# Kernel tuning notes

Measured on AMD Instinct MI355X. Metric: run time of the kernel, lower is better.

The kernel has to match this reference:

```python
import jax, jax.numpy as jnp
import numpy as np

B, N = 64, 4096          # trees per batch, leaves per complete binary tree
V, S = 21, 50            # amino-acid vocab, grammar-symbol vocab
E, H = 64, 128           # embed_dim, hidden_dim


def setup_inputs() -> dict:
    key = jax.random.key(0)
    ks = jax.random.split(key, 16)

    def lin_w(k, din, dout):
        return (jax.random.normal(k, (dout, din), jnp.float32) / np.sqrt(din)).astype(jnp.float32)

    tokens = jax.random.randint(ks[0], (B, N), 0, V, dtype=jnp.int32)
    symbols = jax.random.randint(ks[1], (B, N - 1), 0, S, dtype=jnp.int32)

    emb = jax.random.normal(ks[2], (V, E), jnp.float32) * 0.02
    emb = emb.at[0].set(0.0)  # padding_idx=0
    sym_emb = jax.random.normal(ks[3], (S, E), jnp.float32) * 0.02

    return {
        "tokens": tokens, "symbols": symbols,
        "emb": emb, "sym_emb": sym_emb,
        "Wp": lin_w(ks[4], E, H), "bp": jnp.zeros((H,), jnp.float32),
        "Wi": lin_w(ks[5], H, H), "bi": jnp.zeros((H,), jnp.float32),
        "Ui": lin_w(ks[6], H, H),
        "Wf": lin_w(ks[7], H, H), "bf": jnp.zeros((H,), jnp.float32),
        "Uf": lin_w(ks[8], H, H),
        "Wo": lin_w(ks[9], H, H), "bo": jnp.zeros((H,), jnp.float32),
        "Uo": lin_w(ks[10], H, H),
        "Wu": lin_w(ks[11], H, H), "bu": jnp.zeros((H,), jnp.float32),
        "Uu": lin_w(ks[12], H, H),
        "Wout": lin_w(ks[13], H, H), "bout": jnp.zeros((H,), jnp.float32),
    }


def _encode(tokens, symbols, emb, sym_emb, Wp, bp, Wi, bi, Ui, Wf, bf, Uf,
            Wo, bo, Uo, Wu, bu, Uu, Wout, bout):
    emb = emb.at[0].set(0.0)  # padding row contributes nothing (and gets no grad)

    # Leaf nodes: amino-acid embedding -> input_proj, no children.
    x = emb[tokens] @ Wp.T + bp                      # [B, N, H]
    i = jax.nn.sigmoid(x @ Wi.T + bi)
    o = jax.nn.sigmoid(x @ Wo.T + bo)
    u = jnp.tanh(x @ Wu.T + bu)
    c = i * u                                        # [B, N, H]
    h = o * jnp.tanh(c)

    # Bottom-up over levels of the complete binary tree (Child-Sum Tree-LSTM).
    off, n = 0, N
    while n > 1:
        m = n // 2
        xs = sym_emb[symbols[:, off:off + m]] @ Wp.T + bp   # [B, m, H]
        hl, hr = h[:, 0::2], h[:, 1::2]
        cl, cr = c[:, 0::2], c[:, 1::2]
        ht = hl + hr                                         # h_tilde = sum_j h_j
        gi = jax.nn.sigmoid(xs @ Wi.T + bi + ht @ Ui.T)
        go = jax.nn.sigmoid(xs @ Wo.T + bo + ht @ Uo.T)
        gu = jnp.tanh(xs @ Wu.T + bu + ht @ Uu.T)
        fx = xs @ Wf.T + bf
        fl = jax.nn.sigmoid(fx + hl @ Uf.T)                  # per-child forget gates
        fr = jax.nn.sigmoid(fx + hr @ Uf.T)
        c = gi * gu + fl * cl + fr * cr
        h = go * jnp.tanh(c)
        off += m
        n = m

    root_h = h[:, 0]                                         # [B, H]
    return root_h @ Wout.T + bout                            # output_proj


def reference(tokens, symbols, emb, sym_emb, Wp, bp, Wi, bi, Ui, Wf, bf, Uf,
              Wo, bo, Uo, Wu, bu, Uu, Wout, bout):
    return _encode(tokens, symbols, emb, sym_emb, Wp, bp, Wi, bi, Ui, Wf, bf,
                   Uf, Wo, bo, Uo, Wu, bu, Uu, Wout, bout)
```

## Files before the change

### kernel.cpp

```cpp
#include <hip/hip_runtime.h>
#include <hip/hip_bf16.h>

typedef __attribute__((ext_vector_type(8))) short short8;
typedef __attribute__((ext_vector_type(4))) float f32x4;

static constexpr int B_ = 64;
static constexpr int N_ = 4096;
static constexpr int V_ = 21;
static constexpr int S_ = 50;
static constexpr int E_ = 64;
static constexpr int H_ = 128;
static constexpr int NPAIR = V_ * V_;
static constexpr int NTAB = NPAIR * S_;

__device__ __forceinline__ float rcp_(float x) { return __builtin_amdgcn_rcpf(x); }
__device__ __forceinline__ float sigm(float x) { return rcp_(1.0f + __expf(-x)); }
__device__ __forceinline__ float tanh_(float x) {
  float a = fabsf(x);
  float e = __expf(-2.0f * a);
  float t = (1.0f - e) * rcp_(1.0f + e);
  return x < 0.0f ? -t : t;
}
__device__ __forceinline__ unsigned short f2bf(float f) {
  __hip_bfloat16 b = __float2bfloat16(f);
  return *reinterpret_cast<unsigned short*>(&b);
}
__device__ __forceinline__ float bf2f(unsigned short u) {
  return __uint_as_float(((unsigned int)u) << 16);
}

struct Gates { float cv, hv; };
__device__ __forceinline__ Gates gate_combine(float4 sx,
    float i_p, float o_p, float u_p, float fl_p, float fr_p, float cl, float cr) {
  float gi = sigm(sx.x + i_p);
  float go = sigm(sx.y + o_p);
  float gu = tanh_(sx.z + u_p);
  float fl = sigm(sx.w + fl_p);
  float fr = sigm(sx.w + fr_p);
  float cv = fmaf(gi, gu, fmaf(fl, cl, fr * cr));
  Gates g; g.cv = cv; g.hv = go * tanh_(cv);
  return g;
}

__device__ __forceinline__ void bar_lds() {
  asm volatile("s_waitcnt lgkmcnt(0)" ::: "memory");
  __builtin_amdgcn_s_barrier();
  asm volatile("" ::: "memory");
}
__device__ __forceinline__ void bar_only() {
  asm volatile("" ::: "memory");
  __builtin_amdgcn_s_barrier();
  asm volatile("" ::: "memory");
}

__global__ void __launch_bounds__(512) k_pre(
    const float* __restrict__ Ui, const float* __restrict__ Uo,
    const float* __restrict__ Uu, const float* __restrict__ Uf,
    const float* __restrict__ Wi, const float* __restrict__ Wo,
    const float* __restrict__ Wu, const float* __restrict__ Wf,
    const float* __restrict__ Wp, const float* __restrict__ emb,
    const float* __restrict__ sym_emb,
    const float* __restrict__ bp, const float* __restrict__ bi,
    const float* __restrict__ bo, const float* __restrict__ bu,
    const float* __restrict__ bfv,
    const int* __restrict__ tokens, const int* __restrict__ symbols,
    unsigned short* __restrict__ Wfrag, float* __restrict__ leaf_c,
    float* __restrict__ symx, float* __restrict__ P_leaf,
    int* __restrict__ idx1) {
  __shared__ float x[128];
  __shared__ float zs[512];
  __shared__ float hl[128];
  int blk = blockIdx.x, t = threadIdx.x;
  if (blk < 16) {
    int idx = blk * 512 + t;
    int L = idx & 63;
    int K = (idx >> 6) & 3;
    int T = idx >> 8;
    int n = 16 * T + (L & 15);
    int k0 = 32 * K + ((L >> 4) << 3);
    int g = n >> 7, o = n & 127;
    const float* U = (g == 0) ? Ui : (g == 1) ? Uo : (g == 2) ? Uu : Uf;
    unsigned short out[8];
    #pragma unroll
    for (int j = 0; j < 8; ++j) out[j] = f2bf(U[o * 128 + k0 + j]);
    *(int4*)(Wfrag + (size_t)idx * 8) = *(int4*)out;
  } else if (blk < 16 + V_) {
    int v = blk - 16;
    if (t < 128) {
      float acc = bp[t];
      if (v != 0) {
        const float4* wr = (const float4*)(Wp + t * E_);
        const float4* er = (const float4*)(emb + v * E_);
        #pragma unroll 4
        for (int e4 = 0; e4 < E_ / 4; ++e4) {
          float4 w4 = wr[e4], e4v = er[e4];
          acc = fmaf(e4v.x, w4.x, acc); acc = fmaf(e4v.y, w4.y, acc);
          acc = fmaf(e4v.z, w4.z, acc); acc = fmaf(e4v.w, w4.w, acc);
        }
      }
      x[t] = acc;
    }
    __syncthreads();
    if (t < 384) {
      int g = t >> 7, o = t & 127;
      const float* bb = (g == 0) ? bi : (g == 1) ? bo : bu;
      const float* Wg = (g == 0) ? Wi : (g == 1) ? Wo : Wu;
      float z = bb[o];
      const float4* wr = (const float4*)(Wg + o * H_);
      #pragma unroll 4
      for (int k4 = 0; k4 < H_ / 4; ++k4) {
        float4 w4 = wr[k4];
        z = fmaf(x[4 * k4], w4.x, z); z = fmaf(x[4 * k4 + 1], w4.y, z);
        z = fmaf(x[4 * k4 + 2], w4.z, z); z = fmaf(x[4 * k4 + 3], w4.w, z);
      }
      zs[t] = z;
    }
    __syncthreads();
    if (t < 128) {
      float gi = sigm(zs[t]), go = sigm(zs[128 + t]), gu = tanh_(zs[256 + t]);
      float c = gi * gu;
      leaf_c[v * H_ + t] = c;
      unsigned short hb = f2bf(go * tanh_(c));
      hl[t] = bf2f(hb);
    }
    __syncthreads();
    {
      int g = t >> 7, o = t & 127;
      const float* Ug = (g == 0) ? Ui : (g == 1) ? Uo : (g == 2) ? Uu : Uf;
      float z = 0.f;
      const float4* wr = (const float4*)(Ug + o * H_);
      #pragma unroll 4
      for (int k4 = 0; k4 < H_ / 4; ++k4) {
        float4 w4 = wr[k4];
        z = fmaf(hl[4 * k4], w4.x, z); z = fmaf(hl[4 * k4 + 1], w4.y, z);
        z = fmaf(hl[4 * k4 + 2], w4.z, z); z = fmaf(hl[4 * k4 + 3], w4.w, z);
      }
      P_leaf[(size_t)v * 512 + t] = z;
    }
  } else if (blk < 16 + V_ + S_) {
    int s = blk - 16 - V_;
    if (t < 128) {
      float acc = bp[t];
      const float4* wr = (const float4*)(Wp + t * E_);
      const float4* er = (const float4*)(sym_emb + s * E_);
      #pragma unroll 4
      for (int e4 = 0; e4 < E_ / 4; ++e4) {
        float4 w4 = wr[e4], e4v = er[e4];
        acc = fmaf(e4v.x, w4.x, acc); acc = fmaf(e4v.y, w4.y, acc);
        acc = fmaf(e4v.z, w4.z, acc); acc = fmaf(e4v.w, w4.w, acc);
      }
      x[t] = acc;
    }
    __syncthreads();
    {
      int g = t >> 7, o = t & 127;
      const float* bb = (g == 0) ? bi : (g == 1) ? bo : (g == 2) ? bu : bfv;
      const float* Wg = (g == 0) ? Wi : (g == 1) ? Wo : (g == 2) ? Wu : Wf;
      float z = bb[o];
      const float4* wr = (const float4*)(Wg + o * H_);
      #pragma unroll 4
      for (int k4 = 0; k4 < H_ / 4; ++k4) {
        float4 w4 = wr[k4];
        z = fmaf(x[4 * k4], w4.x, z); z = fmaf(x[4 * k4 + 1], w4.y, z);
        z = fmaf(x[4 * k4 + 2], w4.z, z); z = fmaf(x[4 * k4 + 3], w4.w, z);
      }
      zs[t] = z;
    }
    __syncthreads();
    if (t < 128) {
      float4 v4 = make_float4(zs[t], zs[128 + t], zs[256 + t], zs[384 + t]);
      *(float4*)(symx + (size_t)s * 512 + t * 4) = v4;
    }
  } else {
    int g = (blk - 16 - V_ - S_) * 512 + t;
    int b = g >> 11, j = g & 2047;
    idx1[g] = (tokens[b * N_ + 2 * j] * V_ + tokens[b * N_ + 2 * j + 1]) * S_
              + symbols[b * (N_ - 1) + j];
  }
}

__global__ void k_tabB(const float* __restrict__ P_leaf, const float* __restrict__ symx,
                       const float* __restrict__ leaf_c,
                       unsigned short* __restrict__ tab_h8, float* __restrict__ tab_c) {
  int blk = blockIdx.x, t = threadIdx.x;
  int row = blk * 2 + (t >> 7);
  int u = t & 127;
  int p = row / S_, s = row - p * S_;
  int tl = p / V_, tr = p - tl * V_;
  const float* Pl = P_leaf + (size_t)tl * 512;
  const float* Pr = P_leaf + (size_t)tr * 512;
  float4 sx = *(const float4*)(symx + (size_t)s * 512 + u * 4);
  Gates gt = gate_combine(sx,
      Pl[u] + Pr[u], Pl[128 + u] + Pr[128 + u], Pl[256 + u] + Pr[256 + u],
      Pl[384 + u], Pr[384 + u],
      leaf_c[tl * H_ + u], leaf_c[tr * H_ + u]);
  tab_c[(size_t)row * H_ + u] = gt.cv;
  tab_h8[(size_t)row * H_ + u] = f2bf(gt.hv);
}

__global__ void __launch_bounds__(512) k_lvl23(
    const unsigned short* __restrict__ Wfrag, const float* __restrict__ symx,
    const int* __restrict__ symbols, const int* __restrict__ idx1,
    const unsigned short* __restrict__ gh8, const float* __restrict__ gc,
    unsigned short* __restrict__ h_out8, float* __restrict__ c_out) {
  __shared__ __align__(16) unsigned short Ag[32][136];
  __shared__ __align__(16) unsigned short Bh[16][136];
  __shared__ float Bc[16][132];
  const int t = threadIdx.x;
  const int w = t >> 6, L = t & 63, q = L >> 4, cL = L & 15;
  const int cc = 16 * w + cL;
  const int rowA = t >> 4, coA = (t & 15) * 8;

  const short8* wf = (const short8*)Wfrag;
  short8 bfr[4][4];
  #pragma unroll
  for (int K = 0; K < 4; ++K)
    #pragma unroll
    for (int g = 0; g < 4; ++g)
      bfr[g][K] = wf[(size_t)((w + 8 * g) * 4 + K) * 64 + L];

  const int CH = 8;
  const int t0 = blockIdx.x * CH;

  int nn[4];
  #pragma unroll
  for (int it = 0; it < 4; ++it) nn[it] = 8 * (it >> 1) + 2 * q + (it & 1);

  int gxr = idx1[t0 * 32 + rowA];
  int4 agv = *(const int4*)(gh8 + (size_t)gxr * H_ + coA);
  int g2l[4], g2r[4], sp1[4];
  {
    const int* sb = symbols + (size_t)(t0 >> 6) * (N_ - 1);
    const int j20 = (t0 & 63) * 16;
    #pragma unroll
    for (int it = 0; it < 4; ++it) {
      g2l[it] = idx1[t0 * 32 + 2 * nn[it]];
      g2r[it] = idx1[t0 * 32 + 2 * nn[it] + 1];
      sp1[it] = sb[2048 + j20 + nn[it]];
    }
  }

  for (int k = 0; k < CH; ++k) {
    const int tile = t0 + k;
    const int j2 = (tile & 63) * 16;
    const int* sb = symbols + (size_t)(tile >> 6) * (N_ - 1);

    bar_only();
    *(int4*)&Ag[rowA][coA] = agv;
    bar_lds();

    float clp[4], crp[4];
    #pragma unroll
    for (int it = 0; it < 4; ++it) {
      clp[it] = gc[(size_t)g2l[it] * H_ + cc];
      crp[it] = gc[(size_t)g2r[it] * H_ + cc];
    }
    int gxr_n = 0, g2l_n[4], g2r_n[4], sp1_n[4];
    if (k + 1 < CH) {
      const int tn = tile + 1;
      const int* sbn = symbols + (size_t)(tn >> 6) * (N_ - 1);
      const int j2n = (tn & 63) * 16;
      gxr_n = idx1[tn * 32 + rowA];
      #pragma unroll
      for (int it = 0; it < 4; ++it) {
        g2l_n[it] = idx1[tn * 32 + 2 * nn[it]];
        g2r_n[it] = idx1[tn * 32 + 2 * nn[it] + 1];
        sp1_n[it] = sbn[2048 + j2n + nn[it]];
      }
    }
    int sp2[2];
    sp2[0] = sb[3072 + (j2 >> 1) + 2 * q];
    sp2[1] = sb[3072 + (j2 >> 1) + 2 * q + 1];

    f32x4 acc[2][4];
    #pragma unroll
    for (int r = 0; r < 2; ++r)
      #pragma unroll
      for (int g = 0; g < 4; ++g) acc[r][g] = (f32x4){0.f, 0.f, 0.f, 0.f};
    #pragma unroll
    for (int K = 0; K < 4; ++K) {
      short8 a0 = *(const short8*)&Ag[cL][K * 32 + q * 8];
      short8 a1 = *(const short8*)&Ag[16 + cL][K * 32 + q * 8];
      #pragma unroll
      for (int g = 0; g < 4; ++g) {
        acc[0][g] = __builtin_amdgcn_mfma_f32_16x16x32_bf16(a0, bfr[g][K], acc[0][g], 0, 0, 0);
        acc[1][g] = __builtin_amdgcn_mfma_f32_16x16x32_bf16(a1, bfr[g][K], acc[1][g], 0, 0, 0);
      }
    }
    if (k + 1 < CH) agv = *(const int4*)(gh8 + (size_t)gxr_n * H_ + coA);

    #pragma unroll
    for (int r = 0; r < 2; ++r) {
      #pragma unroll
      for (int nd = 0; nd < 2; ++nd) {
        int it = r * 2 + nd;
        int n = 8 * r + 2 * q + nd;
        float4 sx = *(const float4*)(symx + (size_t)sp1[it] * 512 + cc * 4);
        Gates gt = gate_combine(sx,
            acc[r][0][2 * nd] + acc[r][0][2 * nd + 1],
            acc[r][1][2 * nd] + acc[r][1][2 * nd + 1],
            acc[r][2][2 * nd] + acc[r][2][2 * nd + 1],
            acc[r][3][2 * nd], acc[r][3][2 * nd + 1], clp[it], crp[it]);
        Bc[n][cc] = gt.cv;
        Bh[n][cc] = f2bf(gt.hv);
      }
    }
    bar_lds();

    f32x4 acc2[4];
    #pragma unroll
    for (int g = 0; g < 4; ++g) acc2[g] = (f32x4){0.f, 0.f, 0.f, 0.f};
    #pragma unroll
    for (int K = 0; K < 4; ++K) {
      short8 a0 = *(const short8*)&Bh[cL][K * 32 + q * 8];
      #pragma unroll
      for (int g = 0; g < 4; ++g)
        acc2[g] = __builtin_amdgcn_mfma_f32_16x16x32_bf16(a0, bfr[g][K], acc2[g], 0, 0, 0);
    }
    #pragma unroll
    for (int nd = 0; nd < 2; ++nd) {
      int n = 2 * q + nd;
      int G3 = tile * 8 + n;
      float4 sx = *(const float4*)(symx + (size_t)sp2[nd] * 512 + cc * 4);
      Gates gt = gate_combine(sx,
          acc2[0][2 * nd] + acc2[0][2 * nd + 1],
          acc2[1][2 * nd] + acc2[1][2 * nd + 1],
          acc2[2][2 * nd] + acc2[2][2 * nd + 1],
          acc2[3][2 * nd], acc2[3][2 * nd + 1],
          Bc[2 * n][cc], Bc[2 * n + 1][cc]);
      c_out[(size_t)G3 * H_ + cc] = gt.cv;
      h_out8[(size_t)G3 * H_ + cc] = f2bf(gt.hv);
    }
    gxr = gxr_n;
    #pragma unroll
    for (int it = 0; it < 4; ++it) {
      g2l[it] = g2l_n[it]; g2r[it] = g2r_n[it]; sp1[it] = sp1_n[it];
    }
  }
}

__global__ void __launch_bounds__(512, 2) k_mid(
    const unsigned short* __restrict__ Wfrag, const float* __restrict__ symx,
    const int* __restrict__ symbols,
    const unsigned short* __restrict__ in_h8, const float* __restrict__ in_c,
    unsigned short* __restrict__ out_h8, float* __restrict__ out_c) {
  __shared__ __align__(16) unsigned short Ah0[64][136];
  __shared__ __align__(16) unsigned short Ah1[32][136];
  __shared__ float Cs0[64][128];
  __shared__ float Cs1[32][128];
  int t = threadIdx.x;
  int w = t >> 6, L = t & 63, q = L >> 4, cL = L & 15;
  int cc = 16 * w + cL;
  int blk = blockIdx.x;
  int b = blk >> 3, sub = blk & 7;
  size_t base3 = (size_t)blk * 64;

  #pragma unroll
  for (int i = 0; i < 2; ++i) {
    int fid = t + 512 * i;
    int row = fid >> 4, co = (fid & 15) * 8;
    *(int4*)&Ah0[row][co] = *(const int4*)(in_h8 + (base3 + row) * H_ + co);
  }
  #pragma unroll
  for (int i = 0; i < 4; ++i) {
    int fid = t + 512 * i;
    int row = fid >> 5, c4 = (fid & 31) << 2;
    *(float4*)&Cs0[row][c4] = *(const float4*)(in_c + (base3 + row) * H_ + c4);
  }
  __syncthreads();

  const short8* wf = (const short8*)Wfrag;
  int R = 64;
  #pragma unroll
  for (int lev = 0; lev < 6; ++lev) {
    const int l = 4 + lev;
    const int nodes = R >> 1;
    const int jb = b * (N_ - 1) + (N_ - (N_ >> (l - 1))) + ((sub * 32) >> lev);
    unsigned short (*Ard)[136] = (lev & 1) ? Ah1 : Ah0;
    unsigned short (*Awr)[136] = (lev & 1) ? Ah0 : Ah1;
    const float* crd = (lev & 1) ? &Cs1[0][0] : &Cs0[0][0];
    float* cwr = (lev & 1) ? &Cs0[0][0] : &Cs1[0][0];
    const int nchunk = (nodes + 15) >> 4;
    for (int c = 0; c < nchunk; ++c) {
      int spre[4];
      #pragma unroll
      for (int it = 0; it < 4; ++it) {
        int n = 16 * c + 8 * (it >> 1) + 2 * q + (it & 1);
        spre[it] = (n < nodes) ? symbols[jb + n] : 0;
      }
      f32x4 acc[2][4];
      #pragma unroll
      for (int r = 0; r < 2; ++r)
        #pragma unroll
        for (int g = 0; g < 4; ++g) acc[r][g] = (f32x4){0.f, 0.f, 0.f, 0.f};
      const bool useA1 = (2 * nodes - 32 * c) > 16;
      #pragma unroll
      for (int K = 0; K < 4; ++K) {
        short8 bfr[4];
        #pragma unroll
        for (int g = 0; g < 4; ++g) bfr[g] = wf[(size_t)((w + 8 * g) * 4 + K) * 64 + L];
        short8 a0 = *(const short8*)&Ard[32 * c + cL][K * 32 + q * 8];
        #pragma unroll
        for (int g = 0; g < 4; ++g)
          acc[0][g] = __builtin_amdgcn_mfma_f32_16x16x32_bf16(a0, bfr[g], acc[0][g], 0, 0, 0);
        if (useA1) {
          short8 a1 = *(const short8*)&Ard[32 * c + 16 + cL][K * 32 + q * 8];
          #pragma unroll
          for (int g = 0; g < 4; ++g)
            acc[1][g] = __builtin_amdgcn_mfma_f32_16x16x32_bf16(a1, bfr[g], acc[1][g], 0, 0, 0);
        }
      }
      #pragma unroll
      for (int r = 0; r < 2; ++r) {
        #pragma unroll
        for (int nd = 0; nd < 2; ++nd) {
          int it = r * 2 + nd;
          int n = 16 * c + 8 * r + 2 * q + nd;
          if (n < nodes) {
            float4 sx = *(const float4*)(symx + (size_t)spre[it] * 512 + cc * 4);
            Gates gt = gate_combine(sx,
                acc[r][0][2 * nd] + acc[r][0][2 * nd + 1],
                acc[r][1][2 * nd] + acc[r][1][2 * nd + 1],
                acc[r][2][2 * nd] + acc[r][2][2 * nd + 1],
                acc[r][3][2 * nd], acc[r][3][2 * nd + 1],
                crd[(size_t)(2 * n) * 128 + cc], crd[(size_t)(2 * n + 1) * 128 + cc]);
            if (lev == 5) {
              out_c[(size_t)blk * H_ + cc] = gt.cv;
              out_h8[(size_t)blk * H_ + cc] = f2bf(gt.hv);
            } else {
              cwr[(size_t)n * 128 + cc] = gt.cv;
              Awr[n][cc] = f2bf(gt.hv);
            }
          }
        }
      }
    }
    __syncthreads();
    R >>= 1;
  }
}

__global__ void __launch_bounds__(512, 2) k_fin(
    const unsigned short* __restrict__ Wfrag, const float* __restrict__ symx,
    const int* __restrict__ symbols,
    const unsigned short* __restrict__ in_h8, const float* __restrict__ in_c,
    const float* __restrict__ Wout, const float* __restrict__ bout,
    float* __restrict__ out) {
  __shared__ __align__(16) unsigned short Ah0[8][136];
  __shared__ __align__(16) unsigned short Ah1[4][136];
  __shared__ float Cs0[8][128];
  __shared__ float Cs1[4][128];
  __shared__ float rootv[128];
  int t = threadIdx.x;
  int w = t >> 6, L = t & 63, q = L >> 4, cL = L & 15;
  int cc = 16 * w + cL;
  int b = blockIdx.x;

  if (t < 128) {
    int row = t >> 4, co = (t & 15) * 8;
    *(int4*)&Ah0[row][co] = *(const int4*)(in_h8 + (size_t)(b * 8 + row) * H_ + co);
  }
  if (t < 256) {
    int row = t >> 5, c4 = (t & 31) << 2;
    *(float4*)&Cs0[row][c4] = *(const float4*)(in_c + (size_t)(b * 8 + row) * H_ + c4);
  }
  __syncthreads();

  const short8* wf = (const short8*)Wfrag;
  int R = 8;
  #pragma unroll
  for (int lev = 0; lev < 3; ++lev) {
    const int l = 10 + lev;
    const int nodes = R >> 1;
    const int jb = b * (N_ - 1) + (N_ - (N_ >> (l - 1)));
    unsigned short (*Ard)[136] = (lev & 1) ? Ah1 : Ah0;
    unsigned short (*Awr)[136] = (lev & 1) ? Ah0 : Ah1;
    const float* crd = (lev & 1) ? &Cs1[0][0] : &Cs0[0][0];
    float* cwr = (lev & 1) ? &Cs0[0][0] : &Cs1[0][0];
    int spre[4];
    #pragma unroll
    for (int it = 0; it < 4; ++it) {
      int n = 8 * (it >> 1) + 2 * q + (it & 1);
      spre[it] = (n < nodes) ? symbols[jb + n] : 0;
    }
    f32x4 acc[4];
    #pragma unroll
    for (int g = 0; g < 4; ++g) acc[g] = (f32x4){0.f, 0.f, 0.f, 0.f};
    #pragma unroll
    for (int K = 0; K < 4; ++K) {
      short8 bfr[4];
      #pragma unroll
      for (int g = 0; g < 4; ++g) bfr[g] = wf[(size_t)((w + 8 * g) * 4 + K) * 64 + L];
      short8 a0 = *(const short8*)&Ard[cL & 7][K * 32 + q * 8];
      #pragma unroll
      for (int g = 0; g < 4; ++g)
        acc[g] = __builtin_amdgcn_mfma_f32_16x16x32_bf16(a0, bfr[g], acc[g], 0, 0, 0);
    }
    #pragma unroll
    for (int nd = 0; nd < 2; ++nd) {
      int it = nd;
      int n = 2 * q + nd;
      if (n < nodes) {
        float4 sx = *(const float4*)(symx + (size_t)spre[it] * 512 + cc * 4);
        Gates gt = gate_combine(sx,
            acc[0][2 * nd] + acc[0][2 * nd + 1],
            acc[1][2 * nd] + acc[1][2 * nd + 1],
            acc[2][2 * nd] + acc[2][2 * nd + 1],
            acc[3][2 * nd], acc[3][2 * nd + 1],
            crd[(size_t)(2 * n) * 128 + cc], crd[(size_t)(2 * n + 1) * 128 + cc]);
        if (lev == 2) {
          rootv[cc] = gt.hv;
        } else {
          cwr[(size_t)n * 128 + cc] = gt.cv;
          Awr[n][cc] = f2bf(gt.hv);
        }
      }
    }
    __syncthreads();
    R >>= 1;
  }
  if (t < 128) {
    float acc = bout[t];
    const float4* wr = (const float4*)(Wout + t * H_);
    #pragma unroll 4
    for (int k4 = 0; k4 < H_ / 4; ++k4) {
      float4 w4 = wr[k4];
      acc = fmaf(rootv[4 * k4], w4.x, acc); acc = fmaf(rootv[4 * k4 + 1], w4.y, acc);
      acc = fmaf(rootv[4 * k4 + 2], w4.z, acc); acc = fmaf(rootv[4 * k4 + 3], w4.w, acc);
    }
    out[(size_t)b * H_ + t] = acc;
  }
}

extern "C" void kernel_launch(void* const* d_in, const int* in_sizes, int n_in,
                              void* d_out, int out_size, void* d_ws, size_t ws_size,
                              hipStream_t stream) {
  const int* tokens    = (const int*)d_in[0];
  const int* symbols   = (const int*)d_in[1];
  const float* emb     = (const float*)d_in[2];
  const float* sym_emb = (const float*)d_in[3];
  const float* Wp  = (const float*)d_in[4];
  const float* bp  = (const float*)d_in[5];
  const float* Wi  = (const float*)d_in[6];
  const float* bi  = (const float*)d_in[7];
  const float* Ui  = (const float*)d_in[8];
  const float* Wf  = (const float*)d_in[9];
  const float* bf  = (const float*)d_in[10];
  const float* Uf  = (const float*)d_in[11];
  const float* Wo  = (const float*)d_in[12];
  const float* bo  = (const float*)d_in[13];
  const float* Uo  = (const float*)d_in[14];
  const float* Wu  = (const float*)d_in[15];
  const float* bu  = (const float*)d_in[16];
  const float* Uu  = (const float*)d_in[17];
  const float* Wout= (const float*)d_in[18];
  const float* bout= (const float*)d_in[19];

  char* ws = (char*)d_ws;
  unsigned short* Wfrag   = (unsigned short*)(ws);
  float*          leaf_c  = (float*)(ws + 759040);
  float*          symx    = (float*)(ws + 769792);
  float*          P_leaf  = (float*)(ws + 872192);
  unsigned short* tab_h8  = (unsigned short*)(ws + 2001152UL);
  float*          tab_c   = (float*)(ws + 7645952UL);
  int*            idx1    = (int*)(ws + 18935552UL);
  unsigned short* L3h8    = (unsigned short*)(ws + 19459840UL);
  float*          L3c     = (float*)(ws + 27848448UL);
  unsigned short* L9h8    = (unsigned short*)(ws + 44625664UL);
  float*          L9c     = (float*)(ws + 44756736UL);

  k_pre<<<16 + V_ + S_ + 256, 512, 0, stream>>>(
      Ui, Uo, Uu, Uf, Wi, Wo, Wu, Wf, Wp, emb, sym_emb,
      bp, bi, bo, bu, bf, tokens, symbols,
      Wfrag, leaf_c, symx, P_leaf, idx1);
  k_tabB<<<NTAB / 2, 256, 0, stream>>>(P_leaf, symx, leaf_c, tab_h8, tab_c);
  k_lvl23<<<512, 512, 0, stream>>>(Wfrag, symx, symbols, idx1, tab_h8, tab_c,
                                   L3h8, L3c);
  k_mid<<<512, 512, 0, stream>>>(Wfrag, symx, symbols, L3h8, L3c, L9h8, L9c);
  k_fin<<<B_, 512, 0, stream>>>(Wfrag, symx, symbols, L9h8, L9c, Wout, bout,
                                (float*)d_out);
}
```

Measured before the change: 200.2 us.

## Cut register pressure in tree kernel and hoist weight fragments into registers

In the two-level tile kernel, the cross-iteration prefetch of child indices and symbols is removed and they are now loaded at the point of use. The first MFMA stage runs one 16-row half at a time, so only one set of accumulators is live, which lowers VGPR pressure. The mid and final kernels now load the weight B-fragments into registers once before the level loops instead of reloading them from global memory every chunk and level. Less prefetching exposes more index-load latency, while holding 16 short8 fragments adds registers in the mid and final kernels.

New measurement: 217.5 us. +8.6%, slower.

```diff
diff --git a/kernel.cpp b/kernel.cpp
--- a/kernel.cpp
+++ b/kernel.cpp
@@ -226,81 +226,63 @@
   #pragma unroll
   for (int it = 0; it < 4; ++it) nn[it] = 8 * (it >> 1) + 2 * q + (it & 1);
 
-  int gxr = idx1[t0 * 32 + rowA];
-  int4 agv = *(const int4*)(gh8 + (size_t)gxr * H_ + coA);
-  int g2l[4], g2r[4], sp1[4];
+  int4 agv;
   {
-    const int* sb = symbols + (size_t)(t0 >> 6) * (N_ - 1);
-    const int j20 = (t0 & 63) * 16;
-    #pragma unroll
-    for (int it = 0; it < 4; ++it) {
-      g2l[it] = idx1[t0 * 32 + 2 * nn[it]];
-      g2r[it] = idx1[t0 * 32 + 2 * nn[it] + 1];
-      sp1[it] = sb[2048 + j20 + nn[it]];
-    }
+    int gxr = idx1[t0 * 32 + rowA];
+    agv = *(const int4*)(gh8 + (size_t)gxr * H_ + coA);
   }
 
   for (int k = 0; k < CH; ++k) {
     const int tile = t0 + k;
     const int j2 = (tile & 63) * 16;
     const int* sb = symbols + (size_t)(tile >> 6) * (N_ - 1);
+    const bool hasNext = (k + 1 < CH);
 
     bar_only();
     *(int4*)&Ag[rowA][coA] = agv;
     bar_lds();
 
+    int g2l[4], g2r[4], sp1[4];
+    #pragma unroll
+    for (int it = 0; it < 4; ++it) {
+      g2l[it] = idx1[tile * 32 + 2 * nn[it]];
+      g2r[it] = idx1[tile * 32 + 2 * nn[it] + 1];
+      sp1[it] = sb[2048 + j2 + nn[it]];
+    }
     float clp[4], crp[4];
     #pragma unroll
     for (int it = 0; it < 4; ++it) {
       clp[it] = gc[(size_t)g2l[it] * H_ + cc];
       crp[it] = gc[(size_t)g2r[it] * H_ + cc];
     }
-    int gxr_n = 0, g2l_n[4], g2r_n[4], sp1_n[4];
-    if (k + 1 < CH) {
-      const int tn = tile + 1;
-      const int* sbn = symbols + (size_t)(tn >> 6) * (N_ - 1);
-      const int j2n = (tn & 63) * 16;
-      gxr_n = idx1[tn * 32 + rowA];
-      #pragma unroll
-      for (int it = 0; it < 4; ++it) {
-        g2l_n[it] = idx1[tn * 32 + 2 * nn[it]];
-        g2r_n[it] = idx1[tn * 32 + 2 * nn[it] + 1];
-        sp1_n[it] = sbn[2048 + j2n + nn[it]];
-      }
-    }
     int sp2[2];
     sp2[0] = sb[3072 + (j2 >> 1) + 2 * q];
     sp2[1] = sb[3072 + (j2 >> 1) + 2 * q + 1];
-
-    f32x4 acc[2][4];
-    #pragma unroll
-    for (int r = 0; r < 2; ++r)
-      #pragma unroll
-      for (int g = 0; g < 4; ++g) acc[r][g] = (f32x4){0.f, 0.f, 0.f, 0.f};
-    #pragma unroll
-    for (int K = 0; K < 4; ++K) {
-      short8 a0 = *(const short8*)&Ag[cL][K * 32 + q * 8];
-      short8 a1 = *(const short8*)&Ag[16 + cL][K * 32 + q * 8];
-      #pragma unroll
-      for (int g = 0; g < 4; ++g) {
-        acc[0][g] = __builtin_amdgcn_mfma_f32_16x16x32_bf16(a0, bfr[g][K], acc[0][g], 0, 0, 0);
-        acc[1][g] = __builtin_amdgcn_mfma_f32_16x16x32_bf16(a1, bfr[g][K], acc[1][g], 0, 0, 0);
-      }
-    }
-    if (k + 1 < CH) agv = *(const int4*)(gh8 + (size_t)gxr_n * H_ + coA);
+    int gxr_n = hasNext ? idx1[(tile + 1) * 32 + rowA] : 0;
 
     #pragma unroll
     for (int r = 0; r < 2; ++r) {
+      f32x4 acc[4];
+      #pragma unroll
+      for (int g = 0; g < 4; ++g) acc[g] = (f32x4){0.f, 0.f, 0.f, 0.f};
+      #pragma unroll
+      for (int K = 0; K < 4; ++K) {
+        short8 a = *(const short8*)&Ag[16 * r + cL][K * 32 + q * 8];
+        #pragma unroll
+        for (int g = 0; g < 4; ++g)
+          acc[g] = __builtin_amdgcn_mfma_f32_16x16x32_bf16(a, bfr[g][K], acc[g], 0, 0, 0);
+      }
+      if (r == 0 && hasNext) agv = *(const int4*)(gh8 + (size_t)gxr_n * H_ + coA);
       #pragma unroll
       for (int nd = 0; nd < 2; ++nd) {
-        int it = r * 2 + nd;
+        int it = 2 * r + nd;
         int n = 8 * r + 2 * q + nd;
         float4 sx = *(const float4*)(symx + (size_t)sp1[it] * 512 + cc * 4);
         Gates gt = gate_combine(sx,
-            acc[r][0][2 * nd] + acc[r][0][2 * nd + 1],
-            acc[r][1][2 * nd] + acc[r][1][2 * nd + 1],
-            acc[r][2][2 * nd] + acc[r][2][2 * nd + 1],
-            acc[r][3][2 * nd], acc[r][3][2 * nd + 1], clp[it], crp[it]);
+            acc[0][2 * nd] + acc[0][2 * nd + 1],
+            acc[1][2 * nd] + acc[1][2 * nd + 1],
+            acc[2][2 * nd] + acc[2][2 * nd + 1],
+            acc[3][2 * nd], acc[3][2 * nd + 1], clp[it], crp[it]);
         Bc[n][cc] = gt.cv;
         Bh[n][cc] = f2bf(gt.hv);
       }
@@ -330,11 +312,6 @@
           Bc[2 * n][cc], Bc[2 * n + 1][cc]);
       c_out[(size_t)G3 * H_ + cc] = gt.cv;
       h_out8[(size_t)G3 * H_ + cc] = f2bf(gt.hv);
-    }
-    gxr = gxr_n;
-    #pragma unroll
-    for (int it = 0; it < 4; ++it) {
-      g2l[it] = g2l_n[it]; g2r[it] = g2r_n[it]; sp1[it] = sp1_n[it];
     }
   }
 }
@@ -355,6 +332,14 @@
   int b = blk >> 3, sub = blk & 7;
   size_t base3 = (size_t)blk * 64;
 
+  const short8* wf = (const short8*)Wfrag;
+  short8 bfr[4][4];
+  #pragma unroll
+  for (int K = 0; K < 4; ++K)
+    #pragma unroll
+    for (int g = 0; g < 4; ++g)
+      bfr[g][K] = wf[(size_t)((w + 8 * g) * 4 + K) * 64 + L];
+
   #pragma unroll
   for (int i = 0; i < 2; ++i) {
     int fid = t + 512 * i;
@@ -369,7 +354,6 @@
   }
   __syncthreads();
 
-  const short8* wf = (const short8*)Wfrag;
   int R = 64;
   #pragma unroll
   for (int lev = 0; lev < 6; ++lev) {
@@ -396,18 +380,15 @@
       const bool useA1 = (2 * nodes - 32 * c) > 16;
       #pragma unroll
       for (int K = 0; K < 4; ++K) {
-        short8 bfr[4];
-        #pragma unroll
-        for (int g = 0; g < 4; ++g) bfr[g] = wf[(size_t)((w + 8 * g) * 4 + K) * 64 + L];
         short8 a0 = *(const short8*)&Ard[32 * c + cL][K * 32 + q * 8];
         #pragma unroll
         for (int g = 0; g < 4; ++g)
-          acc[0][g] = __builtin_amdgcn_mfma_f32_16x16x32_bf16(a0, bfr[g], acc[0][g], 0, 0, 0);
+          acc[0][g] = __builtin_amdgcn_mfma_f32_16x16x32_bf16(a0, bfr[g][K], acc[0][g], 0, 0, 0);
         if (useA1) {
           short8 a1 = *(const short8*)&Ard[32 * c + 16 + cL][K * 32 + q * 8];
           #pragma unroll
           for (int g = 0; g < 4; ++g)
-            acc[1][g] = __builtin_amdgcn_mfma_f32_16x16x32_bf16(a1, bfr[g], acc[1][g], 0, 0, 0);
+            acc[1][g] = __builtin_amdgcn_mfma_f32_16x16x32_bf16(a1, bfr[g][K], acc[1][g], 0, 0, 0);
         }
       }
       #pragma unroll
@@ -456,6 +437,14 @@
   int cc = 16 * w + cL;
   int b = blockIdx.x;
 
+  const short8* wf = (const short8*)Wfrag;
+  short8 bfr[4][4];
+  #pragma unroll
+  for (int K = 0; K < 4; ++K)
+    #pragma unroll
+    for (int g = 0; g < 4; ++g)
+      bfr[g][K] = wf[(size_t)((w + 8 * g) * 4 + K) * 64 + L];
+
   if (t < 128) {
     int row = t >> 4, co = (t & 15) * 8;
     *(int4*)&Ah0[row][co] = *(const int4*)(in_h8 + (size_t)(b * 8 + row) * H_ + co);
@@ -466,7 +455,6 @@
   }
   __syncthreads();
 
-  const short8* wf = (const short8*)Wfrag;
   int R = 8;
   #pragma unroll
   for (int lev = 0; lev < 3; ++lev) {
@@ -488,13 +476,10 @@
     for (int g = 0; g < 4; ++g) acc[g] = (f32x4){0.f, 0.f, 0.f, 0.f};
     #pragma unroll
     for (int K = 0; K < 4; ++K) {
-      short8 bfr[4];
-      #pragma unroll
-      for (int g = 0; g < 4; ++g) bfr[g] = wf[(size_t)((w + 8 * g) * 4 + K) * 64 + L];
       short8 a0 = *(const short8*)&Ard[cL & 7][K * 32 + q * 8];
       #pragma unroll
       for (int g = 0; g < 4; ++g)
-        acc[g] = __builtin_amdgcn_mfma_f32_16x16x32_bf16(a0, bfr[g], acc[g], 0, 0, 0);
+        acc[g] = __builtin_amdgcn_mfma_f32_16x16x32_bf16(a0, bfr[g][K], acc[g], 0, 0, 0);
     }
     #pragma unroll
     for (int nd = 0; nd < 2; ++nd) {
```
